# Kernel optimization log

Hardware: AMD Instinct MI355X
Metric: run time of the kernel (lower is better)

Reference implementation:

```python
import jax, jax.numpy as jnp
import numpy as np
from jax import lax

EPSILON = float(np.finfo(np.float32).tiny)
K = 8
TAU = 1.0
HARD = False
B, N = 4096, 8192


def setup_inputs() -> dict:
    key = jax.random.key(0)
    k1, k2 = jax.random.split(key)
    scores = jax.random.normal(k1, (B, N), dtype=jnp.float32)
    # Gumbel(0,1) noise, precomputed for determinism: g = -log(-log(U))
    u = jax.random.uniform(k2, (B, N), dtype=jnp.float32, minval=1e-10, maxval=1.0)
    g = -jnp.log(-jnp.log(u))
    return {"scores": scores, "g": g}


def reference(scores, g):
    s = scores + g  # perturbed logits [B, N]
    khot = jnp.zeros_like(s)
    onehot = jnp.zeros_like(s)

    def step(carry, _):
        s, khot, onehot = carry
        khot_mask = jnp.maximum(1.0 - onehot, EPSILON)
        s = s + jnp.log(khot_mask)
        onehot = jax.nn.softmax(s / TAU, axis=1)
        khot = khot + onehot
        return (s, khot, onehot), None

    (s, khot, onehot), _ = lax.scan(step, (s, khot, onehot), None, length=K)

    if HARD:
        _, ind = lax.top_k(khot, K)  # [B, K]
        khot_hard = jnp.zeros_like(khot).at[jnp.arange(B)[:, None], ind].set(1.0)
        return khot_hard - lax.stop_gradient(khot) + khot
    return khot
```

## Files before the change

### kernel.cpp

```cpp
#include <hip/hip_runtime.h>
#include <math.h>


#define BROWS 4096
#define NCOLS 8192
#define KITER 8
#define THREADS 256
#define VECS 8
#define NWAVES (THREADS / 64)
#define M0 24.0f

typedef float f32x4 __attribute__((ext_vector_type(4)));

__global__ __launch_bounds__(THREADS)
void subset_op_kernel(const float* __restrict__ scores,
                      const float* __restrict__ g,
                      float* __restrict__ out) {
  const int tid = threadIdx.x;
  const int lane = tid & 63;
  const int wave = tid >> 6;
  const long long rbase = (long long)blockIdx.x * NCOLS;

  float w[4 * VECS], kh[4 * VECS];

  float sum = 0.0f;
#pragma unroll
  for (int j = 0; j < VECS; ++j) {
    const int off = j * 1024 + tid * 4;
    const f32x4 sv = *(const f32x4*)(scores + rbase + off);
    const f32x4 gv = *(const f32x4*)(g + rbase + off);
    w[4 * j + 0] = __expf(sv.x + gv.x - M0);
    w[4 * j + 1] = __expf(sv.y + gv.y - M0);
    w[4 * j + 2] = __expf(sv.z + gv.z - M0);
    w[4 * j + 3] = __expf(sv.w + gv.w - M0);
    sum += (w[4 * j + 0] + w[4 * j + 1]) + (w[4 * j + 2] + w[4 * j + 3]);
#pragma unroll
    for (int c = 0; c < 4; ++c) kh[4 * j + c] = 0.0f;
  }

  __shared__ float red[2][NWAVES];

#pragma unroll 1
  for (int k = 0; k < KITER; ++k) {
    float ps = sum;
#pragma unroll
    for (int off = 32; off > 0; off >>= 1) ps += __shfl_xor(ps, off);
    if (lane == 0) red[k & 1][wave] = ps;
    __syncthreads();
    const float tot = (red[k & 1][0] + red[k & 1][1]) +
                      (red[k & 1][2] + red[k & 1][3]);
    const float inv = 1.0f / tot;

    sum = 0.0f;
#pragma unroll
    for (int j = 0; j < 4 * VECS; ++j) {
      const float oh = w[j] * inv;
      kh[j] += oh;
      w[j] = __builtin_fmaf(-oh, w[j], w[j]);
      sum += w[j];
    }
  }

#pragma unroll
  for (int j = 0; j < VECS; ++j) {
    const int off = j * 1024 + tid * 4;
    f32x4 v;
    v.x = kh[4 * j + 0]; v.y = kh[4 * j + 1];
    v.z = kh[4 * j + 2]; v.w = kh[4 * j + 3];
    __builtin_nontemporal_store(v, (f32x4*)(out + rbase + off));
  }
}

extern "C" void kernel_launch(void* const* d_in, const int* in_sizes, int n_in,
                              void* d_out, int out_size, void* d_ws, size_t ws_size,
                              hipStream_t stream) {
  const float* scores = (const float*)d_in[0];
  const float* g = (const float*)d_in[1];
  float* out = (float*)d_out;
  (void)in_sizes; (void)n_in; (void)out_size; (void)d_ws; (void)ws_size;

  subset_op_kernel<<<BROWS, THREADS, 0, stream>>>(scores, g, out);
}
```

Baseline: 69.06 us.

## Process two rows per block and prefetch next row during softmax iterations

```diff
diff --git a/kernel.cpp b/kernel.cpp
--- a/kernel.cpp
+++ b/kernel.cpp
@@ -6,11 +6,14 @@
 #define NCOLS 8192
 #define KITER 8
 #define THREADS 256
+#define RPB 2
+#define GRID (BROWS / RPB)
 #define VECS 8
 #define NWAVES (THREADS / 64)
 #define M0 24.0f
 
 typedef float f32x4 __attribute__((ext_vector_type(4)));
+typedef float f32x2 __attribute__((ext_vector_type(2)));
 
 __global__ __launch_bounds__(THREADS)
 void subset_op_kernel(const float* __restrict__ scores,
@@ -19,55 +22,88 @@
   const int tid = threadIdx.x;
   const int lane = tid & 63;
   const int wave = tid >> 6;
-  const long long rbase = (long long)blockIdx.x * NCOLS;
-
-  float w[4 * VECS], kh[4 * VECS];
-
-  float sum = 0.0f;
-#pragma unroll
-  for (int j = 0; j < VECS; ++j) {
-    const int off = j * 1024 + tid * 4;
-    const f32x4 sv = *(const f32x4*)(scores + rbase + off);
-    const f32x4 gv = *(const f32x4*)(g + rbase + off);
-    w[4 * j + 0] = __expf(sv.x + gv.x - M0);
-    w[4 * j + 1] = __expf(sv.y + gv.y - M0);
-    w[4 * j + 2] = __expf(sv.z + gv.z - M0);
-    w[4 * j + 3] = __expf(sv.w + gv.w - M0);
-    sum += (w[4 * j + 0] + w[4 * j + 1]) + (w[4 * j + 2] + w[4 * j + 3]);
-#pragma unroll
-    for (int c = 0; c < 4; ++c) kh[4 * j + c] = 0.0f;
-  }
+  const long long row0 = (long long)blockIdx.x * RPB;
 
   __shared__ float red[2][NWAVES];
 
-#pragma unroll 1
-  for (int k = 0; k < KITER; ++k) {
-    float ps = sum;
+  f32x4 st[VECS];
+  {
+    const long long rbase = row0 * NCOLS;
 #pragma unroll
-    for (int off = 32; off > 0; off >>= 1) ps += __shfl_xor(ps, off);
-    if (lane == 0) red[k & 1][wave] = ps;
-    __syncthreads();
-    const float tot = (red[k & 1][0] + red[k & 1][1]) +
-                      (red[k & 1][2] + red[k & 1][3]);
-    const float inv = 1.0f / tot;
-
-    sum = 0.0f;
-#pragma unroll
-    for (int j = 0; j < 4 * VECS; ++j) {
-      const float oh = w[j] * inv;
-      kh[j] += oh;
-      w[j] = __builtin_fmaf(-oh, w[j], w[j]);
-      sum += w[j];
+    for (int j = 0; j < VECS; ++j) {
+      const int off = j * 1024 + tid * 4;
+      const f32x4 sv = *(const f32x4*)(scores + rbase + off);
+      const f32x4 gv = *(const f32x4*)(g + rbase + off);
+      st[j] = sv + gv;
     }
   }
 
 #pragma unroll
-  for (int j = 0; j < VECS; ++j) {
-    const int off = j * 1024 + tid * 4;
-    f32x4 v;
-    v.x = kh[4 * j + 0]; v.y = kh[4 * j + 1];
-    v.z = kh[4 * j + 2]; v.w = kh[4 * j + 3];
-    __builtin_nontemporal_store(v, (f32x4*)(out + rbase + off));
+  for (int r = 0; r < RPB; ++r) {
+    f32x2 w2[2 * VECS], kh2[2 * VECS];
+    f32x2 acc0 = {0.0f, 0.0f}, acc1 = {0.0f, 0.0f};
+#pragma unroll
+    for (int j = 0; j < VECS; ++j) {
+      f32x2 lo, hi;
+      lo.x = __expf(st[j].x - M0); lo.y = __expf(st[j].y - M0);
+      hi.x = __expf(st[j].z - M0); hi.y = __expf(st[j].w - M0);
+      w2[2 * j] = lo;  w2[2 * j + 1] = hi;
+      kh2[2 * j] = (f32x2){0.0f, 0.0f};
+      kh2[2 * j + 1] = (f32x2){0.0f, 0.0f};
+      acc0 += lo; acc1 += hi;
+    }
+    const f32x2 accv = acc0 + acc1;
+    float sum = accv.x + accv.y;
+
+    if (r + 1 < RPB) {
+      const long long rbase = (row0 + r + 1) * NCOLS;
+#pragma unroll
+      for (int j = 0; j < VECS; ++j) {
+        const int off = j * 1024 + tid * 4;
+        const f32x4 sv = *(const f32x4*)(scores + rbase + off);
+        const f32x4 gv = *(const f32x4*)(g + rbase + off);
+        st[j] = sv + gv;
+      }
+    }
+
+#pragma unroll 1
+    for (int k = 0; k < KITER; ++k) {
+      float ps = sum;
+#pragma unroll
+      for (int off = 32; off > 0; off >>= 1) ps += __shfl_xor(ps, off);
+      if (lane == 0) red[k & 1][wave] = ps;
+      __syncthreads();
+      const float tot = (red[k & 1][0] + red[k & 1][1]) +
+                        (red[k & 1][2] + red[k & 1][3]);
+      const float inv = 1.0f / tot;
+
+      f32x2 s0 = {0.0f, 0.0f}, s1 = {0.0f, 0.0f};
+      f32x2 s2 = {0.0f, 0.0f}, s3 = {0.0f, 0.0f};
+#pragma unroll
+      for (int j = 0; j < 2 * VECS; ++j) {
+        const f32x2 oh = w2[j] * inv;
+        kh2[j] += oh;
+        w2[j] = __builtin_elementwise_fma(-oh, w2[j], w2[j]);
+        if ((j & 3) == 0)      s0 += w2[j];
+        else if ((j & 3) == 1) s1 += w2[j];
+        else if ((j & 3) == 2) s2 += w2[j];
+        else                   s3 += w2[j];
+      }
+      const f32x2 sv2 = (s0 + s1) + (s2 + s3);
+      sum = sv2.x + sv2.y;
+    }
+
+    {
+      const long long rbase = (row0 + r) * NCOLS;
+#pragma unroll
+      for (int j = 0; j < VECS; ++j) {
+        const int off = j * 1024 + tid * 4;
+        f32x4 v;
+        v.x = kh2[2 * j].x;     v.y = kh2[2 * j].y;
+        v.z = kh2[2 * j + 1].x; v.w = kh2[2 * j + 1].y;
+        __builtin_nontemporal_store(v, (f32x4*)(out + rbase + off));
+      }
+    }
   }
 }
 
@@ -79,5 +115,5 @@
   float* out = (float*)d_out;
   (void)in_sizes; (void)n_in; (void)out_size; (void)d_ws; (void)ws_size;
 
-  subset_op_kernel<<<BROWS, THREADS, 0, stream>>>(scores, g, out);
+  subset_op_kernel<<<GRID, THREADS, 0, stream>>>(scores, g, out);
 }
```

Result: slower. 70.60 us (+2.2%).
